# Kernel tuning notes

Hardware: AMD Instinct MI355X
Metric: run time of the kernel (lower is better)

## Reference

```python
import jax, jax.numpy as jnp
import numpy as np

ENCODER_DIM = 2048
DECODER_DIM = 512
ATTENTION_DIM = 512
BATCH = 512
NUM_PIXELS = 196


def setup_inputs() -> dict:
    key = jax.random.key(0)
    k = jax.random.split(key, 8)
    s_e = 1.0 / np.sqrt(ENCODER_DIM)
    s_d = 1.0 / np.sqrt(DECODER_DIM)
    s_a = 1.0 / np.sqrt(ATTENTION_DIM)
    return {
        "encoder_out": jax.random.normal(k[0], (BATCH, NUM_PIXELS, ENCODER_DIM), jnp.float32),
        "decoder_hidden": jax.random.normal(k[1], (BATCH, DECODER_DIM), jnp.float32),
        "W_enc": jax.random.uniform(k[2], (ENCODER_DIM, ATTENTION_DIM), jnp.float32, -s_e, s_e),
        "b_enc": jax.random.uniform(k[3], (ATTENTION_DIM,), jnp.float32, -s_e, s_e),
        "W_dec": jax.random.uniform(k[4], (DECODER_DIM, ATTENTION_DIM), jnp.float32, -s_d, s_d),
        "b_dec": jax.random.uniform(k[5], (ATTENTION_DIM,), jnp.float32, -s_d, s_d),
        "W_full": jax.random.uniform(k[6], (ATTENTION_DIM,), jnp.float32, -s_a, s_a),
        "b_full": jax.random.uniform(k[7], (), jnp.float32, -s_a, s_a),
    }


def reference(encoder_out, decoder_hidden, W_enc, b_enc, W_dec, b_dec, W_full, b_full):
    # att1: [B, P, A], att2: [B, A]
    att1 = jnp.einsum('bpe,ea->bpa', encoder_out, W_enc) + b_enc
    att2 = decoder_hidden @ W_dec + b_dec
    # scores: [B, P]
    scores = jnp.einsum('bpa,a->bp', jnp.tanh(att1 + att2[:, None, :]), W_full) + b_full
    alpha = jax.nn.softmax(scores, axis=1)
    context = jnp.einsum('bpe,bp->be', encoder_out, alpha)
    return context, alpha
```

## Files before the change

### kernel.cpp

```cpp
#include <hip/hip_runtime.h>
#include <hip/hip_bf16.h>
#include <stdint.h>

#define BATCH 512
#define PIX   196
#define EDIM  2048
#define DDIM  512
#define ADIM  512
#define MROWS (BATCH*PIX)

#define BM 128
#define BN 128
#define BK 32
#define NT (EDIM/BK)

typedef __attribute__((ext_vector_type(8))) short bf16x8;
typedef __attribute__((ext_vector_type(8))) float f32x8;
typedef __attribute__((ext_vector_type(8))) __bf16 bf16v8;
typedef __attribute__((ext_vector_type(4))) float f32x4;

#define GLL16(g, lptr) __builtin_amdgcn_global_load_lds( \
    (const __attribute__((address_space(1))) void*)(g),  \
    (__attribute__((address_space(3))) void*)(lptr), 16, 0, 0)

static __device__ __forceinline__ unsigned short f2bf(float f) {
  union { float f; uint32_t u; } v; v.f = f;
  uint32_t u = v.u;
  return (unsigned short)((u + 0x7FFFu + ((u >> 16) & 1u)) >> 16);
}

static __device__ __forceinline__ float bf2f(unsigned short u) {
  union { uint32_t u; float f; } v; v.u = ((uint32_t)u) << 16;
  return v.f;
}

static __device__ __forceinline__ bf16x8 cvt8(float4 a, float4 b) {
  f32x8 v = {a.x, a.y, a.z, a.w, b.x, b.y, b.z, b.w};
  bf16v8 c = __builtin_convertvector(v, bf16v8);
  bf16x8 r;
  __builtin_memcpy(&r, &c, 16);
  return r;
}

static __device__ __forceinline__ float tanh_fast(float x) {
  const float e = __expf(2.0f * x);
  const float r = __builtin_amdgcn_rcpf(1.0f + e);
  return __builtin_fmaf(-2.0f, r, 1.0f);
}

__global__ void k_transpose_wenc(const float* __restrict__ W,
                                 unsigned short* __restrict__ Bt) {
  __shared__ float tile[32][33];
  const int kt = blockIdx.x;
  const int nt = blockIdx.y;
  const int tx = threadIdx.x, ty = threadIdx.y;
#pragma unroll
  for (int j = 0; j < 4; j++)
    tile[ty + 8*j][tx] = W[(size_t)(kt*32 + ty + 8*j)*ADIM + nt*32 + tx];
  __syncthreads();
#pragma unroll
  for (int j = 0; j < 4; j++)
    Bt[(size_t)(nt*32 + ty + 8*j)*EDIM + kt*32 + tx] = f2bf(tile[tx][ty + 8*j]);
}

__global__ void k_att2p(const float* __restrict__ H, const float* __restrict__ Wd,
                        const float* __restrict__ bd, const float* __restrict__ be,
                        float* __restrict__ att2p) {
  __shared__ float h[DDIM];
  const int b = blockIdx.x;
  const int t = threadIdx.x;
  h[t]       = H[(size_t)b*DDIM + t];
  h[t + 256] = H[(size_t)b*DDIM + t + 256];
  __syncthreads();
  float a0 = 0.f, a1 = 0.f;
#pragma unroll 8
  for (int k = 0; k < DDIM; k++) {
    const float hv = h[k];
    a0 += hv * Wd[(size_t)k*ADIM + t];
    a1 += hv * Wd[(size_t)k*ADIM + t + 256];
  }
  att2p[(size_t)b*ADIM + t]       = a0 + bd[t]       + be[t];
  att2p[(size_t)b*ADIM + t + 256] = a1 + bd[t + 256] + be[t + 256];
}

__global__ __launch_bounds__(256) void k_preconvert(const float* __restrict__ in,
                                                    unsigned short* __restrict__ out,
                                                    long n8) {
  long i = (long)blockIdx.x * 256 + threadIdx.x;
  const long stride = (long)gridDim.x * 256;
  for (; i < n8; i += stride) {
    const float4* p = (const float4*)(in + i*8);
    const float4 a = p[0], b = p[1];
    *(bf16x8*)(out + i*8) = cvt8(a, b);
  }
}

__global__ __launch_bounds__(256, 3) void k_gemm_bf16(
    const unsigned short* __restrict__ At,
    const unsigned short* __restrict__ Bt,
    const float* __restrict__ att2p,
    const float* __restrict__ W_full,
    float* __restrict__ scores)
{
  __shared__ __align__(16) char ldsA[2*8192];
  __shared__ __align__(16) char ldsB[2*8192];
  __shared__ float a2s[2][128];

  const int t   = threadIdx.x;
  const int l   = t & 63;
  const int wid = t >> 6;
  const int wr  = wid >> 1;
  const int wc  = wid & 1;

  const int orig = blockIdx.x;
  const int tile = (orig & 7) * 392 + (orig >> 3);
  const int bm0 = (tile >> 2) * BM;
  const int bn0 = (tile & 3) * BN;

  const int ab0 = bm0 / 196;
  const int ab1 = (bm0 + BM - 1) / 196;
  {
    const int slot = t >> 7, c = t & 127;
    a2s[slot][c] = att2p[(size_t)(slot ? ab1 : ab0) * ADIM + bn0 + c];
  }

  const int r0 = t >> 2, c0 = t & 3;
  const int cswz = (c0 ^ ((r0 >> 1) & 3)) * 8;
  const unsigned short* srcA0 = At + (size_t)(bm0 + r0      ) * EDIM + cswz;
  const unsigned short* srcA1 = At + (size_t)(bm0 + r0 + 64 ) * EDIM + cswz;
  const unsigned short* srcB0 = Bt + (size_t)(bn0 + r0      ) * EDIM + cswz;
  const unsigned short* srcB1 = Bt + (size_t)(bn0 + r0 + 64 ) * EDIM + cswz;
  const int d0 = wid * 1024;
  const int d1 = 4096 + wid * 1024;

  const int l15 = l & 15, hi = l >> 4;
  const int ck  = (hi ^ ((l15 >> 1) & 3)) * 16;
  const int baseA = wr*4096 + l15*64 + ck;
  const int baseB = wc*4096 + l15*64 + ck;

  f32x4 acc[4][4] = {};

#define STG(BUF, KT) do {                                        \
    GLL16(srcA0 + (size_t)(KT)*BK, ldsA + (BUF)*8192 + d0);      \
    GLL16(srcA1 + (size_t)(KT)*BK, ldsA + (BUF)*8192 + d1);      \
    GLL16(srcB0 + (size_t)(KT)*BK, ldsB + (BUF)*8192 + d0);      \
    GLL16(srcB1 + (size_t)(KT)*BK, ldsB + (BUF)*8192 + d1);      \
  } while (0)

#define CMP(BUF) do {                                            \
    bf16x8 af[4], bfr[4];                                        \
    _Pragma("unroll")                                            \
    for (int ni = 0; ni < 4; ni++)                               \
      bfr[ni] = *(const bf16x8*)(ldsB + (BUF)*8192 + ni*1024 + baseB); \
    _Pragma("unroll")                                            \
    for (int mi = 0; mi < 4; mi++)                               \
      af[mi] = *(const bf16x8*)(ldsA + (BUF)*8192 + mi*1024 + baseA); \
    _Pragma("unroll")                                            \
    for (int mi = 0; mi < 4; mi++)                               \
      _Pragma("unroll")                                          \
      for (int ni = 0; ni < 4; ni++)                             \
        acc[mi][ni] = __builtin_amdgcn_mfma_f32_16x16x32_bf16(   \
            af[mi], bfr[ni], acc[mi][ni], 0, 0, 0);              \
  } while (0)

  STG(0, 0);
  __syncthreads();
  for (int kt = 0; kt < NT; kt += 2) {
    STG(1, kt + 1);
    CMP(0);
    __syncthreads();
    if (kt + 2 < NT) STG(0, kt + 2);
    CMP(1);
    __syncthreads();
  }

  float wf[4];
  int cidx[4];
#pragma unroll
  for (int ni = 0; ni < 4; ni++) {
    cidx[ni] = wc*64 + ni*16 + l15;
    wf[ni] = W_full[bn0 + cidx[ni]];
  }
#pragma unroll
  for (int mi = 0; mi < 4; mi++) {
#pragma unroll
    for (int e = 0; e < 4; e++) {
      const int row_l = wr*64 + mi*16 + hi*4 + e;
      const unsigned gr = (unsigned)(bm0 + row_l);
      const int slot = (int)(gr / 196u) - ab0;
      float s = 0.f;
#pragma unroll
      for (int ni = 0; ni < 4; ni++) {
        const float v = acc[mi][ni][e] + a2s[slot][cidx[ni]];
        s += tanh_fast(v) * wf[ni];
      }
      s += __shfl_xor(s, 1); s += __shfl_xor(s, 2);
      s += __shfl_xor(s, 4); s += __shfl_xor(s, 8);
      if (l15 == 0) atomicAdd(&scores[gr], s);
    }
  }
}

__global__ void k_softmax(float* __restrict__ sa) {
  __shared__ float red[256];
  const int b = blockIdx.x, t = threadIdx.x;
  const float v = (t < PIX) ? sa[(size_t)b*PIX + t] : -1e30f;
  red[t] = v; __syncthreads();
  for (int s2 = 128; s2 > 0; s2 >>= 1) {
    if (t < s2) red[t] = fmaxf(red[t], red[t + s2]);
    __syncthreads();
  }
  const float m = red[0]; __syncthreads();
  const float e = (t < PIX) ? __expf(v - m) : 0.f;
  red[t] = e; __syncthreads();
  for (int s2 = 128; s2 > 0; s2 >>= 1) {
    if (t < s2) red[t] += red[t + s2];
    __syncthreads();
  }
  const float inv = 1.f / red[0];
  if (t < PIX) sa[(size_t)b*PIX + t] = e * inv;
}

__global__ __launch_bounds__(256) void k_context_bf16(
    const unsigned short* __restrict__ encbf, const float* __restrict__ alpha,
    float* __restrict__ ctx) {
  __shared__ float al[PIX];
  const int b = blockIdx.x, t = threadIdx.x;
  if (t < PIX) al[t] = alpha[(size_t)b*PIX + t];
  __syncthreads();
  const unsigned short* e = encbf + (size_t)b * PIX * EDIM + t * 8;
  float acc[8] = {};
  for (int p = 0; p < PIX; p++) {
    const bf16x8 v = *(const bf16x8*)(e + (size_t)p * EDIM);
    const float a = al[p];
#pragma unroll
    for (int j = 0; j < 8; j++)
      acc[j] += a * bf2f((unsigned short)v[j]);
  }
  float4 o0 = {acc[0], acc[1], acc[2], acc[3]};
  float4 o1 = {acc[4], acc[5], acc[6], acc[7]};
  float4* dst = (float4*)(ctx + (size_t)b * EDIM + t * 8);
  dst[0] = o0; dst[1] = o1;
}

__global__ __launch_bounds__(256, 3) void k_gemm_scores(
    const float* __restrict__ enc, const unsigned short* __restrict__ Bt,
    const float* __restrict__ att2p, const float* __restrict__ W_full,
    float* __restrict__ scores) {
  __shared__ __align__(16) char ldsA[2*8192];
  __shared__ __align__(16) char ldsB[3*8192];
  __shared__ float a2s[2][128];
  const int t = threadIdx.x, l = t & 63, wid = t >> 6;
  const int wr = wid >> 1, wc = wid & 1;
  const int orig = blockIdx.x;
  const int tile = (orig & 7) * 392 + (orig >> 3);
  const int bm0 = (tile >> 2) * BM, bn0 = (tile & 3) * BN;
  const int ab0 = bm0 / 196;
  const int ab1 = (bm0 + BM - 1) / 196;
  {
    const int slot = t >> 7, c = t & 127;
    a2s[slot][c] = att2p[(size_t)(slot ? ab1 : ab0) * ADIM + bn0 + c];
  }
  const int arow = t >> 1;
  const float* srcA = enc + (size_t)(bm0 + arow) * EDIM + (t & 1) * 16;
  const int g0 = (t & 1) * 2;
  const int wA0 = arow*64 + (((g0    ) ^ ((arow >> 1) & 3)) * 16);
  const int wA1 = arow*64 + (((g0 + 1) ^ ((arow >> 1) & 3)) * 16);
  const unsigned short* srcB[2];
#pragma unroll
  for (int j = 0; j < 2; j++) {
    const int idx = j*256 + t; const int row = idx >> 2;
    srcB[j] = Bt + (size_t)(bn0 + row) * EDIM + ((idx & 3) ^ ((row >> 1) & 3)) * 8;
  }
  const int dB = wid * 1024;
  const int l15 = l & 15, hi = l >> 4;
  const int ck = (hi ^ ((l15 >> 1) & 3)) * 16;
  const int baseA = wr*4096 + l15*64 + ck;
  const int baseB = wc*4096 + l15*64 + ck;
  float4 ar[2][4];
  f32x4 acc[4][4] = {};
#define F_A_ISSUE(SLOT, KT) do { const float* _s = srcA + (size_t)(KT) * BK; \
    ar[SLOT][0] = *(const float4*)(_s); ar[SLOT][1] = *(const float4*)(_s + 4); \
    ar[SLOT][2] = *(const float4*)(_s + 8); ar[SLOT][3] = *(const float4*)(_s + 12); } while (0)
#define F_B_GLL(BUF, KT) do { \
    GLL16(srcB[0] + (size_t)(KT)*BK, ldsB + (BUF)*8192 + dB); \
    GLL16(srcB[1] + (size_t)(KT)*BK, ldsB + (BUF)*8192 + 4096 + dB); } while (0)
#define F_A_WRITE(LBUF, SLOT) do { \
    bf16x8 w0 = cvt8(ar[SLOT][0], ar[SLOT][1]); bf16x8 w1 = cvt8(ar[SLOT][2], ar[SLOT][3]); \
    *(bf16x8*)(ldsA + (LBUF)*8192 + wA0) = w0; *(bf16x8*)(ldsA + (LBUF)*8192 + wA1) = w1; } while (0)
#define F_COMPUTE(BA, BB) do { bf16x8 af[4], bfr[4]; \
    _Pragma("unroll") for (int ni = 0; ni < 4; ni++) \
      bfr[ni] = *(const bf16x8*)(ldsB + (BB)*8192 + ni*1024 + baseB); \
    _Pragma("unroll") for (int mi = 0; mi < 4; mi++) \
      af[mi] = *(const bf16x8*)(ldsA + (BA)*8192 + mi*1024 + baseA); \
    _Pragma("unroll") for (int mi = 0; mi < 4; mi++) \
      _Pragma("unroll") for (int ni = 0; ni < 4; ni++) \
        acc[mi][ni] = __builtin_amdgcn_mfma_f32_16x16x32_bf16(af[mi], bfr[ni], acc[mi][ni], 0, 0, 0); } while (0)
#define F_TILE(T, CUR, BB, BBS) do { F_A_ISSUE(CUR, (T)+2); F_B_GLL(BBS, (T)+2); \
    F_COMPUTE(CUR, BB); asm volatile("s_waitcnt vmcnt(6)" ::: "memory"); \
    F_A_WRITE((CUR)^1, (CUR)^1); asm volatile("s_waitcnt lgkmcnt(0)" ::: "memory"); \
    __builtin_amdgcn_s_barrier(); } while (0)
  F_A_ISSUE(0, 0); F_B_GLL(0, 0); F_A_ISSUE(1, 1); F_B_GLL(1, 1);
  asm volatile("s_waitcnt vmcnt(8)" ::: "memory");
  F_A_WRITE(0, 0);
  asm volatile("s_waitcnt vmcnt(6) lgkmcnt(0)" ::: "memory");
  __builtin_amdgcn_s_barrier();
  for (int kb = 0; kb < 60; kb += 6) {
    F_TILE(kb+0, 0, 0, 2); F_TILE(kb+1, 1, 1, 0); F_TILE(kb+2, 0, 2, 1);
    F_TILE(kb+3, 1, 0, 2); F_TILE(kb+4, 0, 1, 0); F_TILE(kb+5, 1, 2, 1);
  }
  F_TILE(60, 0, 0, 2); F_TILE(61, 1, 1, 0);
  { F_COMPUTE(0, 2); asm volatile("s_waitcnt vmcnt(2)" ::: "memory");
    F_A_WRITE(1, 1); asm volatile("s_waitcnt vmcnt(0) lgkmcnt(0)" ::: "memory");
    __builtin_amdgcn_s_barrier(); }
  F_COMPUTE(1, 0);
  float wf[4]; int cidx[4];
#pragma unroll
  for (int ni = 0; ni < 4; ni++) {
    cidx[ni] = wc*64 + ni*16 + l15;
    wf[ni] = W_full[bn0 + cidx[ni]];
  }
#pragma unroll
  for (int mi = 0; mi < 4; mi++) {
#pragma unroll
    for (int e = 0; e < 4; e++) {
      const int row_l = wr*64 + mi*16 + hi*4 + e;
      const unsigned gr = (unsigned)(bm0 + row_l);
      const int slot = (int)(gr / 196u) - ab0;
      float s = 0.f;
#pragma unroll
      for (int ni = 0; ni < 4; ni++) {
        const float v = acc[mi][ni][e] + a2s[slot][cidx[ni]];
        s += tanh_fast(v) * wf[ni];
      }
      s += __shfl_xor(s, 1); s += __shfl_xor(s, 2);
      s += __shfl_xor(s, 4); s += __shfl_xor(s, 8);
      if (l15 == 0) atomicAdd(&scores[gr], s);
    }
  }
}

__global__ __launch_bounds__(512) void k_context(
    const float* __restrict__ enc, const float* __restrict__ alpha,
    float* __restrict__ ctx) {
  __shared__ float al[PIX];
  const int b = blockIdx.x, t = threadIdx.x;
  if (t < PIX) al[t] = alpha[(size_t)b*PIX + t];
  __syncthreads();
  const float4* e4 = (const float4*)(enc + (size_t)b * PIX * EDIM);
  float4 acc = {0.f, 0.f, 0.f, 0.f};
#pragma unroll 4
  for (int p = 0; p < PIX; p++) {
    const float4 v = e4[(size_t)p * (EDIM/4) + t];
    const float a = al[p];
    acc.x += v.x * a; acc.y += v.y * a; acc.z += v.z * a; acc.w += v.w * a;
  }
  ((float4*)(ctx + (size_t)b * EDIM))[t] = acc;
}

extern "C" void kernel_launch(void* const* d_in, const int* in_sizes, int n_in,
                              void* d_out, int out_size, void* d_ws, size_t ws_size,
                              hipStream_t stream) {
  (void)in_sizes; (void)n_in; (void)out_size;
  const float* enc   = (const float*)d_in[0];
  const float* hid   = (const float*)d_in[1];
  const float* Wenc  = (const float*)d_in[2];
  const float* benc  = (const float*)d_in[3];
  const float* Wdec  = (const float*)d_in[4];
  const float* bdec  = (const float*)d_in[5];
  const float* Wfull = (const float*)d_in[6];

  float* ctx   = (float*)d_out;
  float* alpha = (float*)d_out + (size_t)BATCH * EDIM;

  const size_t encbf_b = (size_t)MROWS * EDIM * 2;
  const size_t bt_b    = (size_t)ADIM * EDIM * 2;
  const size_t att2_b  = (size_t)BATCH * ADIM * 4;

  if (ws_size >= encbf_b + bt_b + att2_b) {
    unsigned short* encbf = (unsigned short*)d_ws;
    unsigned short* Bt    = (unsigned short*)((char*)d_ws + encbf_b);
    float*          att2p = (float*)((char*)d_ws + encbf_b + bt_b);

    hipMemsetAsync(alpha, 0, (size_t)MROWS * sizeof(float), stream);
    k_transpose_wenc<<<dim3(64, 16), dim3(32, 8), 0, stream>>>(Wenc, Bt);
    k_att2p<<<BATCH, 256, 0, stream>>>(hid, Wdec, bdec, benc, att2p);
    k_preconvert<<<2048, 256, 0, stream>>>(enc, encbf, (long)MROWS * EDIM / 8);
    k_gemm_bf16<<<3136, 256, 0, stream>>>(encbf, Bt, att2p, Wfull, alpha);
    k_softmax<<<BATCH, 256, 0, stream>>>(alpha);
    k_context_bf16<<<BATCH, 256, 0, stream>>>(encbf, alpha, ctx);
  } else {
    unsigned short* Bt    = (unsigned short*)d_ws;
    float*          att2p = (float*)((char*)d_ws + bt_b);

    hipMemsetAsync(alpha, 0, (size_t)MROWS * sizeof(float), stream);
    k_transpose_wenc<<<dim3(64, 16), dim3(32, 8), 0, stream>>>(Wenc, Bt);
    k_att2p<<<BATCH, 256, 0, stream>>>(hid, Wdec, bdec, benc, att2p);
    k_gemm_scores<<<3136, 256, 0, stream>>>(enc, Bt, att2p, Wfull, alpha);
    k_softmax<<<BATCH, 256, 0, stream>>>(alpha);
    k_context<<<BATCH, 512, 0, stream>>>(enc, alpha, ctx);
  }
}
```

Measured before the change: 627.3 us.

## Triple-buffer bf16 GEMM LDS pipeline and fuse softmax into context kernel

```diff
diff --git a/kernel.cpp b/kernel.cpp
--- a/kernel.cpp
+++ b/kernel.cpp
@@ -102,8 +102,8 @@
     const float* __restrict__ W_full,
     float* __restrict__ scores)
 {
-  __shared__ __align__(16) char ldsA[2*8192];
-  __shared__ __align__(16) char ldsB[2*8192];
+  __shared__ __align__(16) char ldsA[3*8192];
+  __shared__ __align__(16) char ldsB[3*8192];
   __shared__ float a2s[2][128];
 
   const int t   = threadIdx.x;
@@ -163,16 +163,29 @@
             af[mi], bfr[ni], acc[mi][ni], 0, 0, 0);              \
   } while (0)
 
+#define TILE(T, BUF, BUF2) do {                                  \
+    STG(BUF2, (T)+2);                                            \
+    CMP(BUF);                                                    \
+    asm volatile("s_waitcnt vmcnt(4)" ::: "memory");             \
+    __builtin_amdgcn_s_barrier();                                \
+  } while (0)
+
   STG(0, 0);
-  __syncthreads();
-  for (int kt = 0; kt < NT; kt += 2) {
-    STG(1, kt + 1);
-    CMP(0);
-    __syncthreads();
-    if (kt + 2 < NT) STG(0, kt + 2);
-    CMP(1);
-    __syncthreads();
-  }
+  STG(1, 1);
+  asm volatile("s_waitcnt vmcnt(4)" ::: "memory");
+  __builtin_amdgcn_s_barrier();
+
+  for (int kb = 0; kb < 60; kb += 3) {
+    TILE(kb,     0, 2);
+    TILE(kb + 1, 1, 0);
+    TILE(kb + 2, 2, 1);
+  }
+  TILE(60, 0, 2);
+  TILE(61, 1, 0);
+  CMP(2);
+  asm volatile("s_waitcnt vmcnt(0)" ::: "memory");
+  __builtin_amdgcn_s_barrier();
+  CMP(0);
 
   float wf[4];
   int cidx[4];
@@ -201,6 +214,50 @@
   }
 }
 
+__global__ __launch_bounds__(256) void k_smctx_bf16(
+    const unsigned short* __restrict__ encbf,
+    float* __restrict__ sa,
+    float* __restrict__ ctx) {
+  __shared__ float red[256];
+  __shared__ float al[PIX];
+  const int b = blockIdx.x, t = threadIdx.x;
+
+  const float v = (t < PIX) ? sa[(size_t)b*PIX + t] : -1e30f;
+  red[t] = v; __syncthreads();
+  for (int s2 = 128; s2 > 0; s2 >>= 1) {
+    if (t < s2) red[t] = fmaxf(red[t], red[t + s2]);
+    __syncthreads();
+  }
+  const float m = red[0]; __syncthreads();
+  const float e = (t < PIX) ? __expf(v - m) : 0.f;
+  red[t] = e; __syncthreads();
+  for (int s2 = 128; s2 > 0; s2 >>= 1) {
+    if (t < s2) red[t] += red[t + s2];
+    __syncthreads();
+  }
+  const float inv = 1.f / red[0];
+  if (t < PIX) {
+    const float a = e * inv;
+    al[t] = a;
+    sa[(size_t)b*PIX + t] = a;
+  }
+  __syncthreads();
+
+  const unsigned short* ep = encbf + (size_t)b * PIX * EDIM + t * 8;
+  float acc[8] = {};
+  for (int p = 0; p < PIX; p++) {
+    const bf16x8 vv = *(const bf16x8*)(ep + (size_t)p * EDIM);
+    const float a = al[p];
+#pragma unroll
+    for (int j = 0; j < 8; j++)
+      acc[j] += a * bf2f((unsigned short)vv[j]);
+  }
+  float4 o0 = {acc[0], acc[1], acc[2], acc[3]};
+  float4 o1 = {acc[4], acc[5], acc[6], acc[7]};
+  float4* dst = (float4*)(ctx + (size_t)b * EDIM + t * 8);
+  dst[0] = o0; dst[1] = o1;
+}
+
 __global__ void k_softmax(float* __restrict__ sa) {
   __shared__ float red[256];
   const int b = blockIdx.x, t = threadIdx.x;
@@ -219,28 +276,6 @@
   }
   const float inv = 1.f / red[0];
   if (t < PIX) sa[(size_t)b*PIX + t] = e * inv;
-}
-
-__global__ __launch_bounds__(256) void k_context_bf16(
-    const unsigned short* __restrict__ encbf, const float* __restrict__ alpha,
-    float* __restrict__ ctx) {
-  __shared__ float al[PIX];
-  const int b = blockIdx.x, t = threadIdx.x;
-  if (t < PIX) al[t] = alpha[(size_t)b*PIX + t];
-  __syncthreads();
-  const unsigned short* e = encbf + (size_t)b * PIX * EDIM + t * 8;
-  float acc[8] = {};
-  for (int p = 0; p < PIX; p++) {
-    const bf16x8 v = *(const bf16x8*)(e + (size_t)p * EDIM);
-    const float a = al[p];
-#pragma unroll
-    for (int j = 0; j < 8; j++)
-      acc[j] += a * bf2f((unsigned short)v[j]);
-  }
-  float4 o0 = {acc[0], acc[1], acc[2], acc[3]};
-  float4 o1 = {acc[4], acc[5], acc[6], acc[7]};
-  float4* dst = (float4*)(ctx + (size_t)b * EDIM + t * 8);
-  dst[0] = o0; dst[1] = o1;
 }
 
 __global__ __launch_bounds__(256, 3) void k_gemm_scores(
@@ -387,8 +422,7 @@
     k_att2p<<<BATCH, 256, 0, stream>>>(hid, Wdec, bdec, benc, att2p);
     k_preconvert<<<2048, 256, 0, stream>>>(enc, encbf, (long)MROWS * EDIM / 8);
     k_gemm_bf16<<<3136, 256, 0, stream>>>(encbf, Bt, att2p, Wfull, alpha);
-    k_softmax<<<BATCH, 256, 0, stream>>>(alpha);
-    k_context_bf16<<<BATCH, 256, 0, stream>>>(encbf, alpha, ctx);
+    k_smctx_bf16<<<BATCH, 256, 0, stream>>>(encbf, alpha, ctx);
   } else {
     unsigned short* Bt    = (unsigned short*)d_ws;
     float*          att2p = (float*)((char*)d_ws + bt_b);
```

After: 618.9 us. No clear change (-1.3%).
